# Kernel tuning notes

Hardware: AMD Instinct MI355X
Metric: run time of the kernel (lower is better)

The kernel has to match this reference:

```python
import jax, jax.numpy as jnp
import numpy as np


def lga_once(x, w, r):
    """One pass of local guided aggregation (GANet LGA).

    x: [B, D, H, W] cost volume
    w: [B, 3*k*k, H, W] per-pixel guidance weights (k = 2r+1); the three
       k*k groups weight disparity planes d, d-1, d+1 respectively.
    out[b,d,h,w] = sum_{i,j in kxk window}
        w0[b,ij,h,w] * x[b, d,   h+i-r, w+j-r]
      + w1[b,ij,h,w] * x[b, d-1, h+i-r, w+j-r]
      + w2[b,ij,h,w] * x[b, d+1, h+i-r, w+j-r]
    with zero padding outside spatial and disparity bounds.
    """
    B, D, H, W = x.shape
    k = 2 * r + 1
    k2 = k * k
    w0 = w[:, 0 * k2:1 * k2]
    w1 = w[:, 1 * k2:2 * k2]
    w2 = w[:, 2 * k2:3 * k2]
    # disparity-shifted volumes: xm[:, d] = x[:, d-1], xp[:, d] = x[:, d+1]
    xm = jnp.pad(x, ((0, 0), (1, 0), (0, 0), (0, 0)))[:, :D]
    xp = jnp.pad(x, ((0, 0), (0, 1), (0, 0), (0, 0)))[:, 1:]
    spad = ((0, 0), (0, 0), (r, r), (r, r))
    x0p = jnp.pad(x, spad)
    xmp = jnp.pad(xm, spad)
    xpp = jnp.pad(xp, spad)
    out = jnp.zeros_like(x)
    idx = 0
    for i in range(k):          # small fixed kxk loop; data dims stay vectorized
        for j in range(k):
            p0 = x0p[:, :, i:i + H, j:j + W]
            pm = xmp[:, :, i:i + H, j:j + W]
            pp = xpp[:, :, i:i + H, j:j + W]
            out = out + (w0[:, idx:idx + 1] * p0
                         + w1[:, idx:idx + 1] * pm
                         + w2[:, idx:idx + 1] * pp)
            idx += 1
    return out


def setup_inputs() -> dict:
    key = jax.random.key(0)
    k1, k2 = jax.random.split(key)
    B, D, H, W = 2, 48, 320, 640
    r = 2
    kk = 2 * r + 1
    input1 = jax.random.normal(k1, (B, D, H, W), dtype=jnp.float32)
    input2 = jax.random.uniform(k2, (B, 3 * kk * kk, H, W), dtype=jnp.float32)
    return {"input1": input1, "input2": input2, "radius": r}


def reference(input1, input2, radius):
    # LGA2 = local guided aggregation applied twice with the same weights
    y = lga_once(input1, input2, radius)
    return lga_once(y, input2, radius)
```

## Files before the change

kernel.cpp:

```cpp
#include <hip/hip_runtime.h>

namespace {
constexpr int Bn = 2, Dn = 48, Hn = 320, Wn = 640;
constexpr int R = 2, K = 5, K2 = 25, C3 = 75;
constexpr int TW = 64, TH = 4;
constexpr int LW = TW + 2 * R;
constexpr int NT = TW * TH;
constexpr int LTOT = 544;
constexpr int SPAD = 640;
constexpr int NSLOT = 6;
}

#define BARRIER(N) \
    asm volatile("s_waitcnt vmcnt(" #N ") lgkmcnt(0)\n\ts_barrier" ::: "memory")

__global__ __launch_bounds__(NT, 2)
void lga_pass(const float* __restrict__ x, const float* __restrict__ wt,
              float* __restrict__ out) {
    __shared__ float2 pl2[NSLOT][SPAD];

    const int tx = threadIdx.x;
    const int ty = threadIdx.y;

    const int w0pix = blockIdx.x * TW;
    const int h0pix = blockIdx.y * TH;
    const int b = blockIdx.z;

    const int gw = w0pix + tx;
    const int gh = h0pix + ty;

    const size_t ps = (size_t)Hn * Wn;

    int soffA[5];
#pragma unroll
    for (int t = 0; t < 5; ++t) {
        int s = ty * 160 + t * 32 + (tx >> 1);
        int rr = s / LW;
        int cc = s - rr * LW;
        int hh = h0pix - R + rr;
        int ww = w0pix - R + cc;
        bool ok = (s < LTOT) && hh >= 0 && hh < Hn && ww >= 0 && ww < Wn;
        soffA[t] = ok ? (hh * Wn + ww) : 0;
    }

    const float* xb = x + (size_t)b * Dn * ps;
    const float* xq = xb + (size_t)(tx & 1) * ps;

    float wr[C3];
    {
        const float* wp = wt + (size_t)b * C3 * ps + (size_t)gh * Wn + gw;
#pragma unroll
        for (int c = 0; c < C3; ++c) wr[c] = wp[(size_t)c * ps];
#pragma unroll
        for (int i = 0; i < K; ++i) {
            const int hh = gh + i - R;
            const bool vh = (hh >= 0) && (hh < Hn);
#pragma unroll
            for (int j = 0; j < K; ++j) {
                const int ww = gw + j - R;
                if (!(vh && ww >= 0 && ww < Wn)) {
                    wr[i * K + j] = 0.f;
                    wr[K2 + i * K + j] = 0.f;
                    wr[2 * K2 + i * K + j] = 0.f;
                }
            }
        }
    }

    float* op = out + (size_t)b * Dn * ps + (size_t)gh * Wn + gw;
    const int lbase = ty * LW + tx;

    auto dma = [&](const float* pbase, int slot) {
#pragma unroll
        for (int t = 0; t < 5; ++t) {
            __builtin_amdgcn_global_load_lds(
                (const __attribute__((address_space(1))) void*)(pbase + soffA[t]),
                (__attribute__((address_space(3))) void*)(&pl2[slot][ty * 160 + t * 32]),
                4, 0, 0);
        }
    };

    float carry = 0.f, s1prev = 0.f;
    const float* pref = xq;

    dma(pref, 0); pref += 2 * ps;
    dma(pref, 1); pref += 2 * ps;
    dma(pref, 2); pref += 2 * ps;

    auto stepc = [&](int slot, bool issue, bool first) {
        if (issue) { dma(pref, (slot + 3 >= NSLOT) ? slot - 3 : slot + 3); pref += 2 * ps; }
        float S0a = 0.f, S1a = 0.f, S2a = 0.f;
        float S0b = 0.f, S1b = 0.f, S2b = 0.f;
        const float2* wb = &pl2[slot][lbase];
#pragma unroll
        for (int i = 0; i < K; ++i)
#pragma unroll
            for (int j = 0; j < K; ++j) {
                float2 v = wb[i * LW + j];
                float w0 = wr[i * K + j];
                float w1 = wr[K2 + i * K + j];
                float w2 = wr[2 * K2 + i * K + j];
                S0a += w0 * v.x; S1a += w1 * v.x; S2a += w2 * v.x;
                S0b += w0 * v.y; S1b += w1 * v.y; S2b += w2 * v.y;
            }
        if (first) op[(size_t)(Dn - 1) * ps] = carry + S2a;
        else       { *op = carry + S2a; op += ps; }
        carry = S0a + s1prev; s1prev = S1a;
        *op = carry + S2b; op += ps;
        carry = S0b + s1prev; s1prev = S1b;
    };

    BARRIER(10); stepc(0, true, true);
    BARRIER(12); stepc(1, true, false);
    BARRIER(14); stepc(2, true, false);
    for (int g = 0; g < 3; ++g) {
        BARRIER(16); stepc(3, true, false);
        BARRIER(16); stepc(4, true, false);
        BARRIER(16); stepc(5, true, false);
        BARRIER(16); stepc(0, true, false);
        BARRIER(16); stepc(1, true, false);
        BARRIER(16); stepc(2, true, false);
    }
    BARRIER(16); stepc(3, false, false);
    BARRIER(11); stepc(4, false, false);
    BARRIER(6);  stepc(5, false, false);
    *op = carry;
}

extern "C" void kernel_launch(void* const* d_in, const int* in_sizes, int n_in,
                              void* d_out, int out_size, void* d_ws, size_t ws_size,
                              hipStream_t stream) {
    const float* x = (const float*)d_in[0];
    const float* w = (const float*)d_in[1];
    float* out = (float*)d_out;
    float* tmp = (float*)d_ws;

    dim3 block(TW, TH, 1);
    dim3 grid(Wn / TW, Hn / TH, Bn);

    lga_pass<<<grid, block, 0, stream>>>(x, w, tmp);
    lga_pass<<<grid, block, 0, stream>>>(tmp, w, out);
}
```

Before: 457.6 us.

## Replace LDS DMA pipeline with direct per-thread global loads of clamped windows

```diff
diff --git a/kernel.cpp b/kernel.cpp
--- a/kernel.cpp
+++ b/kernel.cpp
@@ -4,126 +4,91 @@
 constexpr int Bn = 2, Dn = 48, Hn = 320, Wn = 640;
 constexpr int R = 2, K = 5, K2 = 25, C3 = 75;
 constexpr int TW = 64, TH = 4;
-constexpr int LW = TW + 2 * R;
 constexpr int NT = TW * TH;
-constexpr int LTOT = 544;
-constexpr int SPAD = 640;
-constexpr int NSLOT = 6;
 }
-
-#define BARRIER(N) \
-    asm volatile("s_waitcnt vmcnt(" #N ") lgkmcnt(0)\n\ts_barrier" ::: "memory")
 
 __global__ __launch_bounds__(NT, 2)
 void lga_pass(const float* __restrict__ x, const float* __restrict__ wt,
               float* __restrict__ out) {
-    __shared__ float2 pl2[NSLOT][SPAD];
-
     const int tx = threadIdx.x;
     const int ty = threadIdx.y;
 
-    const int w0pix = blockIdx.x * TW;
-    const int h0pix = blockIdx.y * TH;
+    const int gw = blockIdx.x * TW + tx;
+    const int gh = blockIdx.y * TH + ty;
     const int b = blockIdx.z;
-
-    const int gw = w0pix + tx;
-    const int gh = h0pix + ty;
 
     const size_t ps = (size_t)Hn * Wn;
 
-    int soffA[5];
-#pragma unroll
-    for (int t = 0; t < 5; ++t) {
-        int s = ty * 160 + t * 32 + (tx >> 1);
-        int rr = s / LW;
-        int cc = s - rr * LW;
-        int hh = h0pix - R + rr;
-        int ww = w0pix - R + cc;
-        bool ok = (s < LTOT) && hh >= 0 && hh < Hn && ww >= 0 && ww < Wn;
-        soffA[t] = ok ? (hh * Wn + ww) : 0;
-    }
-
-    const float* xb = x + (size_t)b * Dn * ps;
-    const float* xq = xb + (size_t)(tx & 1) * ps;
+    const int cb = min(max(gw - R, 0), Wn - K);
+    const int s = (gw - R) - cb;
 
     float wr[C3];
     {
         const float* wp = wt + (size_t)b * C3 * ps + (size_t)gh * Wn + gw;
 #pragma unroll
-        for (int c = 0; c < C3; ++c) wr[c] = wp[(size_t)c * ps];
-#pragma unroll
         for (int i = 0; i < K; ++i) {
             const int hh = gh + i - R;
             const bool vh = (hh >= 0) && (hh < Hn);
 #pragma unroll
-            for (int j = 0; j < K; ++j) {
-                const int ww = gw + j - R;
-                if (!(vh && ww >= 0 && ww < Wn)) {
-                    wr[i * K + j] = 0.f;
-                    wr[K2 + i * K + j] = 0.f;
-                    wr[2 * K2 + i * K + j] = 0.f;
+            for (int k = 0; k < K; ++k) {
+                const int jj = k - s;
+                const bool ok = vh && (jj >= 0) && (jj < K);
+                const int c = i * K + jj;
+                float w0 = 0.f, w1 = 0.f, w2 = 0.f;
+                if (ok) {
+                    w0 = wp[(size_t)c * ps];
+                    w1 = wp[(size_t)(K2 + c) * ps];
+                    w2 = wp[(size_t)(2 * K2 + c) * ps];
                 }
+                wr[i * K + k] = w0;
+                wr[K2 + i * K + k] = w1;
+                wr[2 * K2 + i * K + k] = w2;
             }
         }
     }
 
+    const float* xb = x + (size_t)b * Dn * ps;
+    const float* p0 = xb + (size_t)min(max(gh - 2, 0), Hn - 1) * Wn + cb;
+    const float* p1 = xb + (size_t)min(max(gh - 1, 0), Hn - 1) * Wn + cb;
+    const float* p2 = xb + (size_t)gh * Wn + cb;
+    const float* p3 = xb + (size_t)min(gh + 1, Hn - 1) * Wn + cb;
+    const float* p4 = xb + (size_t)min(gh + 2, Hn - 1) * Wn + cb;
+
     float* op = out + (size_t)b * Dn * ps + (size_t)gh * Wn + gw;
-    const int lbase = ty * LW + tx;
-
-    auto dma = [&](const float* pbase, int slot) {
-#pragma unroll
-        for (int t = 0; t < 5; ++t) {
-            __builtin_amdgcn_global_load_lds(
-                (const __attribute__((address_space(1))) void*)(pbase + soffA[t]),
-                (__attribute__((address_space(3))) void*)(&pl2[slot][ty * 160 + t * 32]),
-                4, 0, 0);
-        }
-    };
 
     float carry = 0.f, s1prev = 0.f;
-    const float* pref = xq;
 
-    dma(pref, 0); pref += 2 * ps;
-    dma(pref, 1); pref += 2 * ps;
-    dma(pref, 2); pref += 2 * ps;
+#pragma unroll 1
+    for (int d = 0; d < Dn; ++d) {
+        float v[K][K];
+#pragma unroll
+        for (int k = 0; k < K; ++k) v[0][k] = p0[k];
+#pragma unroll
+        for (int k = 0; k < K; ++k) v[1][k] = p1[k];
+#pragma unroll
+        for (int k = 0; k < K; ++k) v[2][k] = p2[k];
+#pragma unroll
+        for (int k = 0; k < K; ++k) v[3][k] = p3[k];
+#pragma unroll
+        for (int k = 0; k < K; ++k) v[4][k] = p4[k];
 
-    auto stepc = [&](int slot, bool issue, bool first) {
-        if (issue) { dma(pref, (slot + 3 >= NSLOT) ? slot - 3 : slot + 3); pref += 2 * ps; }
-        float S0a = 0.f, S1a = 0.f, S2a = 0.f;
-        float S0b = 0.f, S1b = 0.f, S2b = 0.f;
-        const float2* wb = &pl2[slot][lbase];
+        float S0 = 0.f, S1 = 0.f, S2 = 0.f;
 #pragma unroll
         for (int i = 0; i < K; ++i)
 #pragma unroll
-            for (int j = 0; j < K; ++j) {
-                float2 v = wb[i * LW + j];
-                float w0 = wr[i * K + j];
-                float w1 = wr[K2 + i * K + j];
-                float w2 = wr[2 * K2 + i * K + j];
-                S0a += w0 * v.x; S1a += w1 * v.x; S2a += w2 * v.x;
-                S0b += w0 * v.y; S1b += w1 * v.y; S2b += w2 * v.y;
+            for (int k = 0; k < K; ++k) {
+                const float vv = v[i][k];
+                S0 += wr[i * K + k] * vv;
+                S1 += wr[K2 + i * K + k] * vv;
+                S2 += wr[2 * K2 + i * K + k] * vv;
             }
-        if (first) op[(size_t)(Dn - 1) * ps] = carry + S2a;
-        else       { *op = carry + S2a; op += ps; }
-        carry = S0a + s1prev; s1prev = S1a;
-        *op = carry + S2b; op += ps;
-        carry = S0b + s1prev; s1prev = S1b;
-    };
 
-    BARRIER(10); stepc(0, true, true);
-    BARRIER(12); stepc(1, true, false);
-    BARRIER(14); stepc(2, true, false);
-    for (int g = 0; g < 3; ++g) {
-        BARRIER(16); stepc(3, true, false);
-        BARRIER(16); stepc(4, true, false);
-        BARRIER(16); stepc(5, true, false);
-        BARRIER(16); stepc(0, true, false);
-        BARRIER(16); stepc(1, true, false);
-        BARRIER(16); stepc(2, true, false);
+        if (d > 0) { *op = carry + S2; op += ps; }
+        carry = S0 + s1prev;
+        s1prev = S1;
+
+        p0 += ps; p1 += ps; p2 += ps; p3 += ps; p4 += ps;
     }
-    BARRIER(16); stepc(3, false, false);
-    BARRIER(11); stepc(4, false, false);
-    BARRIER(6);  stepc(5, false, false);
     *op = carry;
 }
 
```

Result: slower. 468.0 us (+2.3%).
